# Performance work log

Measured on AMD Instinct MI355X. Metric: run time of the kernel, lower is better.

The kernel has to match this reference:

```python
import jax, jax.numpy as jnp
import numpy as np

DROPOUT_P = 0.0  # undefined global `dropout_p` in source; pinned to 0 (identity) for determinism


def setup_inputs() -> dict:
    key = jax.random.key(0)
    k1, k2, k3 = jax.random.split(key, 3)
    B, Lq, Lk, D = 16, 4096, 4096, 64
    return {
        "query": jax.random.normal(k1, (B, Lq, D), dtype=jnp.float32),
        "key": jax.random.normal(k2, (B, Lk, D), dtype=jnp.float32),
        "value": jax.random.normal(k3, (B, Lk, D), dtype=jnp.float32),
        "scale_factor": jnp.ones((1,), dtype=jnp.float32),
    }


def reference(query, key, value, scale_factor):
    # scores: [B, Lq, Lk] -- the large HBM-materialized intermediate
    scores = jnp.einsum("bqd,bkd->bqk", query, key) / scale_factor
    probs = jax.nn.softmax(scores, axis=-1)
    # dropout with p = DROPOUT_P = 0.0 is the identity
    out = jnp.einsum("bqk,bkd->bqd", probs, value)
    return out
```

## Files before the change

### kernel.cpp

```cpp
#include <hip/hip_runtime.h>
#include <hip/hip_fp16.h>

typedef _Float16 half2_t __attribute__((ext_vector_type(2)));
typedef _Float16 half4_t __attribute__((ext_vector_type(4)));
typedef _Float16 half8_t __attribute__((ext_vector_type(8)));
typedef float   float4_t __attribute__((ext_vector_type(4)));
typedef float  float16_t __attribute__((ext_vector_type(16)));

static __device__ __forceinline__ half2_t cvt_pk(float a, float b) {
    return __builtin_bit_cast(half2_t, __builtin_amdgcn_cvt_pkrtz(a, b));
}
static __device__ __forceinline__ half4_t cvt_pk4(float a, float b, float c, float d) {
    half2_t lo = cvt_pk(a, b), hi = cvt_pk(c, d);
    half4_t r;
    r[0] = lo[0]; r[1] = lo[1]; r[2] = hi[0]; r[3] = hi[1];
    return r;
}
static __device__ __forceinline__ half8_t cvt_pk8(const float4& a, const float4& b) {
    half4_t lo = cvt_pk4(a.x, a.y, a.z, a.w);
    half4_t hi = cvt_pk4(b.x, b.y, b.z, b.w);
    return __builtin_shufflevector(lo, hi, 0, 1, 2, 3, 4, 5, 6, 7);
}
static __device__ __forceinline__ half8_t join8(half4_t lo, half4_t hi) {
    return __builtin_shufflevector(lo, hi, 0, 1, 2, 3, 4, 5, 6, 7);
}
static __device__ __forceinline__ float f3(float a, float b, float c) {
    return fmaxf(fmaxf(a, b), c);
}

namespace {
constexpr int kB       = 16;
constexpr int kL       = 4096;
constexpr int kD       = 64;
constexpr int kQTile   = 128;
constexpr int kBK      = 64;
constexpr int kTiles   = kL / kBK;
constexpr int kSplit   = 2;
constexpr int kTilesHf = kTiles / kSplit;
constexpr int kTileH   = kBK * kD;
constexpr int kKStride = 72;
constexpr int kVStride = 72;
constexpr size_t kWsHalves = (size_t)kB * kTiles * kTileH;
constexpr size_t kOHalves  = (size_t)kB * kL * kD;
}


__global__ __launch_bounds__(256) void prep_kv(const float* __restrict__ K,
                                               const float* __restrict__ V,
                                               _Float16* __restrict__ Kws,
                                               _Float16* __restrict__ Vws)
{
    int blk = blockIdx.x;
    const int tid = threadIdx.x;
    if (blk < kB * kTiles) {
        const float* src = K + (size_t)blk * kTileH;
        _Float16* dst = Kws + (size_t)blk * kTileH;
#pragma unroll
        for (int i = 0; i < 2; ++i) {
            const int task = tid + 256 * i;
            const int row  = task >> 3;
            const int g    = task & 7;
            const int srow = (row & ~12) | ((row & 4) << 1) | ((row & 8) >> 1);
            const float* p = src + srow * kD + g * 8;
            const float4 a  = *(const float4*)p;
            const float4 b2 = *(const float4*)(p + 4);
            *(half8_t*)(dst + task * 8) = cvt_pk8(a, b2);
        }
    } else {
        blk -= kB * kTiles;
        const float* src = V + (size_t)blk * kTileH;
        _Float16* dst = Vws + (size_t)blk * kTileH;
        const int d  = tid & 63;
        const int vw = tid >> 6;
#pragma unroll
        for (int i = 0; i < 2; ++i) {
            const int c8 = vw * 2 + i;
            const int k0 = c8 * 8;
            float p[8];
#pragma unroll
            for (int j = 0; j < 8; ++j) p[j] = src[(k0 + j) * kD + d];
            half4_t lo = cvt_pk4(p[0], p[1], p[2], p[3]);
            half4_t hi = cvt_pk4(p[4], p[5], p[6], p[7]);
            *(half8_t*)(dst + (c8 * 64 + d) * 8) = join8(lo, hi);
        }
    }
}

__global__ __launch_bounds__(256, 4)
void fa_fwd(const float* __restrict__ Q, const _Float16* __restrict__ Kws,
            const _Float16* __restrict__ Vws, const float* __restrict__ scale_ptr,
            float* __restrict__ Out, _Float16* __restrict__ O2ws,
            float* __restrict__ Mlws)
{
    __shared__ __align__(16) _Float16 Ksh[2][kBK * kKStride];
    __shared__ __align__(16) _Float16 Vsh[2][kD * kVStride];

    const int tid  = threadIdx.x;
    const int wave = tid >> 6;
    const int lane = tid & 63;
    const int l31  = lane & 31;
    const int hi   = lane >> 5;

    const int b  = blockIdx.y;
    const int hf = blockIdx.z;
    const int q0 = blockIdx.x * kQTile + wave * 32;

    const int task0 = tid, task1 = tid + 256;
    const int vd = tid & 63;
    const int vw = tid >> 6;
    const int koff0 = (task0 >> 3) * kKStride + (task0 & 7) * 8;
    const int koff1 = (task1 >> 3) * kKStride + (task1 & 7) * 8;
    const int voff0 = vd * kVStride + (vw * 2 + 0) * 8;
    const int voff1 = vd * kVStride + (vw * 2 + 1) * 8;

    const float qscale = 1.4426950408889634f / scale_ptr[0];

    const float*    Qb = Q   + (size_t)b * kL * kD;
    const _Float16* Kt = Kws + ((size_t)b * kTiles + (size_t)hf * kTilesHf) * kTileH;
    const _Float16* Vt = Vws + ((size_t)b * kTiles + (size_t)hf * kTilesHf) * kTileH;

    half8_t qfrag[4];
    {
        const float* qrow = Qb + (size_t)(q0 + l31) * kD;
#pragma unroll
        for (int kd = 0; kd < 4; ++kd) {
            const float* p = qrow + kd * 16 + hi * 8;
            half8_t h;
#pragma unroll
            for (int j = 0; j < 8; ++j) h[j] = (_Float16)(p[j] * qscale);
            qfrag[kd] = h;
        }
    }

    float16_t O[2];
    O[0] = (float16_t)0.0f;
    O[1] = (float16_t)0.0f;
    float m_run = -__builtin_inff();
    float l_run = 0.0f;
    const float16_t Zc = (float16_t)0.0f;

    half8_t kp[2], vp[2];
    kp[0] = *(const half8_t*)(Kt + task0 * 8);
    kp[1] = *(const half8_t*)(Kt + task1 * 8);
    vp[0] = *(const half8_t*)(Vt + ((vw * 2 + 0) * 64 + vd) * 8);
    vp[1] = *(const half8_t*)(Vt + ((vw * 2 + 1) * 64 + vd) * 8);
    *(half8_t*)(&Ksh[0][koff0]) = kp[0];
    *(half8_t*)(&Ksh[0][koff1]) = kp[1];
    *(half8_t*)(&Vsh[0][voff0]) = vp[0];
    *(half8_t*)(&Vsh[0][voff1]) = vp[1];
    {
        const _Float16* kn = Kt + (size_t)1 * kTileH;
        const _Float16* vn = Vt + (size_t)1 * kTileH;
        kp[0] = *(const half8_t*)(kn + task0 * 8);
        kp[1] = *(const half8_t*)(kn + task1 * 8);
        vp[0] = *(const half8_t*)(vn + ((vw * 2 + 0) * 64 + vd) * 8);
        vp[1] = *(const half8_t*)(vn + ((vw * 2 + 1) * 64 + vd) * 8);
    }
    __syncthreads();

    for (int t = 0; t < kTilesHf; ++t) {
        const int cur = t & 1;
        const _Float16* Kb = Ksh[cur];
        const _Float16* Vb = Vsh[cur];
        _Float16* Kn = Ksh[cur ^ 1];
        _Float16* Vn = Vsh[cur ^ 1];

        *(half8_t*)(&Kn[koff0]) = kp[0];
        *(half8_t*)(&Kn[koff1]) = kp[1];
        *(half8_t*)(&Vn[voff0]) = vp[0];
        *(half8_t*)(&Vn[voff1]) = vp[1];

        {
            const int nt = (t + 2) & (kTilesHf - 1);
            const _Float16* kn = Kt + (size_t)nt * kTileH;
            const _Float16* vn = Vt + (size_t)nt * kTileH;
            kp[0] = *(const half8_t*)(kn + task0 * 8);
            kp[1] = *(const half8_t*)(kn + task1 * 8);
            vp[0] = *(const half8_t*)(vn + ((vw * 2 + 0) * 64 + vd) * 8);
            vp[1] = *(const half8_t*)(vn + ((vw * 2 + 1) * 64 + vd) * 8);
        }

        float16_t S0, S1;
        {
            half8_t kf0, kf1;
            kf0 = *(const half8_t*)(&Kb[(l31)      * kKStride + 0 * 16 + hi * 8]);
            kf1 = *(const half8_t*)(&Kb[(32 + l31) * kKStride + 0 * 16 + hi * 8]);
            __builtin_amdgcn_s_setprio(1);
            S0 = __builtin_amdgcn_mfma_f32_32x32x16_f16(kf0, qfrag[0], Zc, 0, 0, 0);
            S1 = __builtin_amdgcn_mfma_f32_32x32x16_f16(kf1, qfrag[0], Zc, 0, 0, 0);
#pragma unroll
            for (int kd = 1; kd < 4; ++kd) {
                kf0 = *(const half8_t*)(&Kb[(l31)      * kKStride + kd * 16 + hi * 8]);
                kf1 = *(const half8_t*)(&Kb[(32 + l31) * kKStride + kd * 16 + hi * 8]);
                S0 = __builtin_amdgcn_mfma_f32_32x32x16_f16(kf0, qfrag[kd], S0, 0, 0, 0);
                S1 = __builtin_amdgcn_mfma_f32_32x32x16_f16(kf1, qfrag[kd], S1, 0, 0, 0);
            }
            __builtin_amdgcn_s_setprio(0);
        }

        float v0 = f3(S0[0],  S0[1],  S0[2]);
        float v1 = f3(S0[3],  S0[4],  S0[5]);
        float v2 = f3(S0[6],  S0[7],  S0[8]);
        float v3 = f3(S0[9],  S0[10], S0[11]);
        float v4 = f3(S0[12], S0[13], S0[14]);
        float v5 = f3(S0[15], S1[0],  S1[1]);
        float v6 = f3(S1[2],  S1[3],  S1[4]);
        float v7 = f3(S1[5],  S1[6],  S1[7]);
        float v8 = f3(S1[8],  S1[9],  S1[10]);
        float v9 = f3(S1[11], S1[12], S1[13]);
        float w0 = f3(v0, v1, v2);
        float w1 = f3(v3, v4, v5);
        float w2 = f3(v6, v7, v8);
        float w3 = f3(v9, S1[14], S1[15]);
        float pm = fmaxf(fmaxf(w0, w1), fmaxf(w2, w3));
        pm = fmaxf(pm, __shfl_xor(pm, 32));

        const bool need = pm > m_run + 8.0f;
        if (__ballot(need)) {
            const float mn    = fmaxf(m_run, pm);
            const float alpha = __builtin_amdgcn_exp2f(m_run - mn);
            m_run = mn;
            l_run *= alpha;
#pragma unroll
            for (int r = 0; r < 16; ++r) { O[0][r] *= alpha; O[1][r] *= alpha; }
        }

#pragma unroll
        for (int r = 0; r < 16; ++r) {
            S0[r] = __builtin_amdgcn_exp2f(S0[r] - m_run);
            S1[r] = __builtin_amdgcn_exp2f(S1[r] - m_run);
        }
        half8_t pf[4];
        pf[0] = join8(cvt_pk4(S0[0],  S0[1],  S0[2],  S0[3]),
                      cvt_pk4(S0[4],  S0[5],  S0[6],  S0[7]));
        pf[1] = join8(cvt_pk4(S0[8],  S0[9],  S0[10], S0[11]),
                      cvt_pk4(S0[12], S0[13], S0[14], S0[15]));
        pf[2] = join8(cvt_pk4(S1[0],  S1[1],  S1[2],  S1[3]),
                      cvt_pk4(S1[4],  S1[5],  S1[6],  S1[7]));
        pf[3] = join8(cvt_pk4(S1[8],  S1[9],  S1[10], S1[11]),
                      cvt_pk4(S1[12], S1[13], S1[14], S1[15]));
#define A4(v,a) ((v[a] + v[(a)+1]) + (v[(a)+2] + v[(a)+3]))
        l_run += ((A4(S0, 0) + A4(S0, 4)) + (A4(S0, 8) + A4(S0, 12)))
               + ((A4(S1, 0) + A4(S1, 4)) + (A4(S1, 8) + A4(S1, 12)));
#undef A4

        __builtin_amdgcn_s_setprio(1);
#pragma unroll
        for (int kb = 0; kb < 4; ++kb) {
            const half8_t vf0 = *(const half8_t*)(
                &Vb[(l31)      * kVStride + kb * 16 + hi * 8]);
            const half8_t vf1 = *(const half8_t*)(
                &Vb[(32 + l31) * kVStride + kb * 16 + hi * 8]);
            O[0] = __builtin_amdgcn_mfma_f32_32x32x16_f16(vf0, pf[kb], O[0], 0, 0, 0);
            O[1] = __builtin_amdgcn_mfma_f32_32x32x16_f16(vf1, pf[kb], O[1], 0, 0, 0);
        }
        __builtin_amdgcn_s_setprio(0);

        __syncthreads();
    }

    l_run += __shfl_xor(l_run, 32);
    const float inv = 1.0f / l_run;
    const int   q   = q0 + l31;
    if (hf == 0) {
        float* op = Out + ((size_t)b * kL + q) * kD;
#pragma unroll
        for (int dt = 0; dt < 2; ++dt)
#pragma unroll
            for (int rr = 0; rr < 4; ++rr) {
                const int d0 = dt * 32 + rr * 8 + hi * 4;
                float4 w;
                w.x = O[dt][rr * 4 + 0] * inv;
                w.y = O[dt][rr * 4 + 1] * inv;
                w.z = O[dt][rr * 4 + 2] * inv;
                w.w = O[dt][rr * 4 + 3] * inv;
                *(float4*)(op + d0) = w;
            }
    } else {
        _Float16* op = O2ws + ((size_t)b * kL + q) * kD;
#pragma unroll
        for (int dt = 0; dt < 2; ++dt)
#pragma unroll
            for (int rr = 0; rr < 4; ++rr) {
                const int d0 = dt * 32 + rr * 8 + hi * 4;
                half4_t w = cvt_pk4(O[dt][rr * 4 + 0] * inv, O[dt][rr * 4 + 1] * inv,
                                    O[dt][rr * 4 + 2] * inv, O[dt][rr * 4 + 3] * inv);
                *(half4_t*)(op + d0) = w;
            }
    }
    if (hi == 0) {
        float2 ml; ml.x = m_run; ml.y = l_run;
        *(float2*)(Mlws + (((size_t)b * kL + q) * 2 + hf) * 2) = ml;
    }
}

__global__ __launch_bounds__(256)
void combine(float* __restrict__ Out, const _Float16* __restrict__ O2ws,
             const float* __restrict__ Mlws)
{
    const int t   = threadIdx.x;
    const int row = blockIdx.x * 16 + (t >> 4);
    const int d0  = (t & 15) * 4;

    const float m1 = Mlws[(size_t)row * 4 + 0];
    const float l1 = Mlws[(size_t)row * 4 + 1];
    const float m2 = Mlws[(size_t)row * 4 + 2];
    const float l2 = Mlws[(size_t)row * 4 + 3];

    const float m  = fmaxf(m1, m2);
    float w1 = l1 * exp2f(m1 - m);
    float w2 = l2 * exp2f(m2 - m);
    const float inv = 1.0f / (w1 + w2);
    w1 *= inv; w2 *= inv;

    float* op = Out + (size_t)row * kD + d0;
    const _Float16* o2 = O2ws + (size_t)row * kD + d0;
    float4 a = *(const float4*)op;
    const half4_t h = *(const half4_t*)o2;
    a.x = a.x * w1 + (float)h[0] * w2;
    a.y = a.y * w1 + (float)h[1] * w2;
    a.z = a.z * w1 + (float)h[2] * w2;
    a.w = a.w * w1 + (float)h[3] * w2;
    *(float4*)op = a;
}

extern "C" void kernel_launch(void* const* d_in, const int* in_sizes, int n_in,
                              void* d_out, int out_size, void* d_ws, size_t ws_size,
                              hipStream_t stream) {
    const float* Q = (const float*)d_in[0];
    const float* K = (const float*)d_in[1];
    const float* V = (const float*)d_in[2];
    const float* s = (const float*)d_in[3];
    float* out = (float*)d_out;
    _Float16* Kws  = (_Float16*)d_ws;
    _Float16* Vws  = Kws + kWsHalves;
    _Float16* O2ws = Vws + kWsHalves;
    float*    Mlws = (float*)(O2ws + kOHalves);

    prep_kv<<<dim3(2 * kB * kTiles), dim3(256), 0, stream>>>(K, V, Kws, Vws);
    fa_fwd<<<dim3(kL / kQTile, kB, kSplit), dim3(256), 0, stream>>>(Q, Kws, Vws, s, out, O2ws, Mlws);
    combine<<<dim3(kB * kL / 16), dim3(256), 0, stream>>>(out, O2ws, Mlws);
}
```

Before: 186.0 us.

## Load V fragments directly from global into registers, drop V LDS staging

V tiles are no longer staged through shared memory. Each wave loads its MFMA B-operand fragments for V straight from the pre-swizzled global workspace at the start of each tile iteration, and these loads are consumed after the QK^T and softmax work. The K LDS store and next-tile prefetch are moved after the QK MFMAs. This halves LDS footprint and LDS traffic, but each of the 4 waves now reads the full V tile from global/L2 (4x redundant), and load latency is only hidden within one iteration.

```diff
diff --git a/kernel.cpp b/kernel.cpp
--- a/kernel.cpp
+++ b/kernel.cpp
@@ -39,7 +39,6 @@
 constexpr int kTilesHf = kTiles / kSplit;
 constexpr int kTileH   = kBK * kD;
 constexpr int kKStride = 72;
-constexpr int kVStride = 72;
 constexpr size_t kWsHalves = (size_t)kB * kTiles * kTileH;
 constexpr size_t kOHalves  = (size_t)kB * kL * kD;
 }
@@ -93,7 +92,6 @@
             float* __restrict__ Mlws)
 {
     __shared__ __align__(16) _Float16 Ksh[2][kBK * kKStride];
-    __shared__ __align__(16) _Float16 Vsh[2][kD * kVStride];
 
     const int tid  = threadIdx.x;
     const int wave = tid >> 6;
@@ -106,12 +104,8 @@
     const int q0 = blockIdx.x * kQTile + wave * 32;
 
     const int task0 = tid, task1 = tid + 256;
-    const int vd = tid & 63;
-    const int vw = tid >> 6;
     const int koff0 = (task0 >> 3) * kKStride + (task0 & 7) * 8;
     const int koff1 = (task1 >> 3) * kKStride + (task1 & 7) * 8;
-    const int voff0 = vd * kVStride + (vw * 2 + 0) * 8;
-    const int voff1 = vd * kVStride + (vw * 2 + 1) * 8;
 
     const float qscale = 1.4426950408889634f / scale_ptr[0];
 
@@ -139,45 +133,27 @@
     float l_run = 0.0f;
     const float16_t Zc = (float16_t)0.0f;
 
-    half8_t kp[2], vp[2];
+    half8_t kp[2];
     kp[0] = *(const half8_t*)(Kt + task0 * 8);
     kp[1] = *(const half8_t*)(Kt + task1 * 8);
-    vp[0] = *(const half8_t*)(Vt + ((vw * 2 + 0) * 64 + vd) * 8);
-    vp[1] = *(const half8_t*)(Vt + ((vw * 2 + 1) * 64 + vd) * 8);
     *(half8_t*)(&Ksh[0][koff0]) = kp[0];
     *(half8_t*)(&Ksh[0][koff1]) = kp[1];
-    *(half8_t*)(&Vsh[0][voff0]) = vp[0];
-    *(half8_t*)(&Vsh[0][voff1]) = vp[1];
-    {
-        const _Float16* kn = Kt + (size_t)1 * kTileH;
-        const _Float16* vn = Vt + (size_t)1 * kTileH;
-        kp[0] = *(const half8_t*)(kn + task0 * 8);
-        kp[1] = *(const half8_t*)(kn + task1 * 8);
-        vp[0] = *(const half8_t*)(vn + ((vw * 2 + 0) * 64 + vd) * 8);
-        vp[1] = *(const half8_t*)(vn + ((vw * 2 + 1) * 64 + vd) * 8);
-    }
+    kp[0] = *(const half8_t*)(Kt + (size_t)kTileH + task0 * 8);
+    kp[1] = *(const half8_t*)(Kt + (size_t)kTileH + task1 * 8);
     __syncthreads();
 
     for (int t = 0; t < kTilesHf; ++t) {
         const int cur = t & 1;
         const _Float16* Kb = Ksh[cur];
-        const _Float16* Vb = Vsh[cur];
         _Float16* Kn = Ksh[cur ^ 1];
-        _Float16* Vn = Vsh[cur ^ 1];
-
-        *(half8_t*)(&Kn[koff0]) = kp[0];
-        *(half8_t*)(&Kn[koff1]) = kp[1];
-        *(half8_t*)(&Vn[voff0]) = vp[0];
-        *(half8_t*)(&Vn[voff1]) = vp[1];
-
-        {
-            const int nt = (t + 2) & (kTilesHf - 1);
-            const _Float16* kn = Kt + (size_t)nt * kTileH;
-            const _Float16* vn = Vt + (size_t)nt * kTileH;
-            kp[0] = *(const half8_t*)(kn + task0 * 8);
-            kp[1] = *(const half8_t*)(kn + task1 * 8);
-            vp[0] = *(const half8_t*)(vn + ((vw * 2 + 0) * 64 + vd) * 8);
-            vp[1] = *(const half8_t*)(vn + ((vw * 2 + 1) * 64 + vd) * 8);
+
+        const _Float16* vtile = Vt + (size_t)t * kTileH;
+        half8_t vr0[4], vr1[4];
+#pragma unroll
+        for (int kb = 0; kb < 4; ++kb) {
+            const _Float16* pch = vtile + (kb * 2 + hi) * 512;
+            vr0[kb] = *(const half8_t*)(pch + l31 * 8);
+            vr1[kb] = *(const half8_t*)(pch + (32 + l31) * 8);
         }
 
         float16_t S0, S1;
@@ -196,6 +172,15 @@
                 S1 = __builtin_amdgcn_mfma_f32_32x32x16_f16(kf1, qfrag[kd], S1, 0, 0, 0);
             }
             __builtin_amdgcn_s_setprio(0);
+        }
+
+        *(half8_t*)(&Kn[koff0]) = kp[0];
+        *(half8_t*)(&Kn[koff1]) = kp[1];
+        {
+            const int nt = (t + 2) & (kTilesHf - 1);
+            const _Float16* kn = Kt + (size_t)nt * kTileH;
+            kp[0] = *(const half8_t*)(kn + task0 * 8);
+            kp[1] = *(const half8_t*)(kn + task1 * 8);
         }
 
         float v0 = f3(S0[0],  S0[1],  S0[2]);
@@ -247,12 +232,8 @@
         __builtin_amdgcn_s_setprio(1);
 #pragma unroll
         for (int kb = 0; kb < 4; ++kb) {
-            const half8_t vf0 = *(const half8_t*)(
-                &Vb[(l31)      * kVStride + kb * 16 + hi * 8]);
-            const half8_t vf1 = *(const half8_t*)(
-                &Vb[(32 + l31) * kVStride + kb * 16 + hi * 8]);
-            O[0] = __builtin_amdgcn_mfma_f32_32x32x16_f16(vf0, pf[kb], O[0], 0, 0, 0);
-            O[1] = __builtin_amdgcn_mfma_f32_32x32x16_f16(vf1, pf[kb], O[1], 0, 0, 0);
+            O[0] = __builtin_amdgcn_mfma_f32_32x32x16_f16(vr0[kb], pf[kb], O[0], 0, 0, 0);
+            O[1] = __builtin_amdgcn_mfma_f32_32x32x16_f16(vr1[kb], pf[kb], O[1], 0, 0, 0);
         }
         __builtin_amdgcn_s_setprio(0);
 
```

New measurement: 231.4 us. +24.4%, slower.

## Software-pipeline PV MFMA of previous tile with QK MFMA of current tile

Applied to the files above, without the earlier changes.

Defers the P·V matrix multiply of each key tile into the next loop iteration, issuing it right after the Q·K^T MFMAs so matrix work overlaps the softmax math. V fragments and packed probabilities are kept in registers across iterations, and a final epilogue flushes the last tile. This aims to hide softmax/exp latency behind MFMA issue, at the cost of extra VGPR pressure that could reduce occupancy.

```diff
diff --git a/kernel.cpp b/kernel.cpp
--- a/kernel.cpp
+++ b/kernel.cpp
@@ -138,6 +138,11 @@
     float m_run = -__builtin_inff();
     float l_run = 0.0f;
     const float16_t Zc = (float16_t)0.0f;
+
+    const half8_t hz = (half8_t)(_Float16)0.0f;
+    half8_t pf[4]  = {hz, hz, hz, hz};
+    half8_t vfr0[4] = {hz, hz, hz, hz};
+    half8_t vfr1[4] = {hz, hz, hz, hz};
 
     half8_t kp[2], vp[2];
     kp[0] = *(const half8_t*)(Kt + task0 * 8);
@@ -165,11 +170,34 @@
         _Float16* Kn = Ksh[cur ^ 1];
         _Float16* Vn = Vsh[cur ^ 1];
 
+        float16_t S0, S1;
+        {
+            half8_t kf0, kf1;
+            kf0 = *(const half8_t*)(&Kb[(l31)      * kKStride + 0 * 16 + hi * 8]);
+            kf1 = *(const half8_t*)(&Kb[(32 + l31) * kKStride + 0 * 16 + hi * 8]);
+            __builtin_amdgcn_s_setprio(1);
+            S0 = __builtin_amdgcn_mfma_f32_32x32x16_f16(kf0, qfrag[0], Zc, 0, 0, 0);
+            S1 = __builtin_amdgcn_mfma_f32_32x32x16_f16(kf1, qfrag[0], Zc, 0, 0, 0);
+#pragma unroll
+            for (int kd = 1; kd < 4; ++kd) {
+                kf0 = *(const half8_t*)(&Kb[(l31)      * kKStride + kd * 16 + hi * 8]);
+                kf1 = *(const half8_t*)(&Kb[(32 + l31) * kKStride + kd * 16 + hi * 8]);
+                S0 = __builtin_amdgcn_mfma_f32_32x32x16_f16(kf0, qfrag[kd], S0, 0, 0, 0);
+                S1 = __builtin_amdgcn_mfma_f32_32x32x16_f16(kf1, qfrag[kd], S1, 0, 0, 0);
+            }
+#pragma unroll
+            for (int kb = 0; kb < 4; ++kb)
+                O[0] = __builtin_amdgcn_mfma_f32_32x32x16_f16(vfr0[kb], pf[kb], O[0], 0, 0, 0);
+#pragma unroll
+            for (int kb = 0; kb < 4; ++kb)
+                O[1] = __builtin_amdgcn_mfma_f32_32x32x16_f16(vfr1[kb], pf[kb], O[1], 0, 0, 0);
+            __builtin_amdgcn_s_setprio(0);
+        }
+
         *(half8_t*)(&Kn[koff0]) = kp[0];
         *(half8_t*)(&Kn[koff1]) = kp[1];
         *(half8_t*)(&Vn[voff0]) = vp[0];
         *(half8_t*)(&Vn[voff1]) = vp[1];
-
         {
             const int nt = (t + 2) & (kTilesHf - 1);
             const _Float16* kn = Kt + (size_t)nt * kTileH;
@@ -178,24 +206,6 @@
             kp[1] = *(const half8_t*)(kn + task1 * 8);
             vp[0] = *(const half8_t*)(vn + ((vw * 2 + 0) * 64 + vd) * 8);
             vp[1] = *(const half8_t*)(vn + ((vw * 2 + 1) * 64 + vd) * 8);
-        }
-
-        float16_t S0, S1;
-        {
-            half8_t kf0, kf1;
-            kf0 = *(const half8_t*)(&Kb[(l31)      * kKStride + 0 * 16 + hi * 8]);
-            kf1 = *(const half8_t*)(&Kb[(32 + l31) * kKStride + 0 * 16 + hi * 8]);
-            __builtin_amdgcn_s_setprio(1);
-            S0 = __builtin_amdgcn_mfma_f32_32x32x16_f16(kf0, qfrag[0], Zc, 0, 0, 0);
-            S1 = __builtin_amdgcn_mfma_f32_32x32x16_f16(kf1, qfrag[0], Zc, 0, 0, 0);
-#pragma unroll
-            for (int kd = 1; kd < 4; ++kd) {
-                kf0 = *(const half8_t*)(&Kb[(l31)      * kKStride + kd * 16 + hi * 8]);
-                kf1 = *(const half8_t*)(&Kb[(32 + l31) * kKStride + kd * 16 + hi * 8]);
-                S0 = __builtin_amdgcn_mfma_f32_32x32x16_f16(kf0, qfrag[kd], S0, 0, 0, 0);
-                S1 = __builtin_amdgcn_mfma_f32_32x32x16_f16(kf1, qfrag[kd], S1, 0, 0, 0);
-            }
-            __builtin_amdgcn_s_setprio(0);
         }
 
         float v0 = f3(S0[0],  S0[1],  S0[2]);
@@ -230,34 +240,37 @@
             S0[r] = __builtin_amdgcn_exp2f(S0[r] - m_run);
             S1[r] = __builtin_amdgcn_exp2f(S1[r] - m_run);
         }
-        half8_t pf[4];
+
         pf[0] = join8(cvt_pk4(S0[0],  S0[1],  S0[2],  S0[3]),
                       cvt_pk4(S0[4],  S0[5],  S0[6],  S0[7]));
         pf[1] = join8(cvt_pk4(S0[8],  S0[9],  S0[10], S0[11]),
                       cvt_pk4(S0[12], S0[13], S0[14], S0[15]));
+#pragma unroll
+        for (int kb = 0; kb < 4; ++kb)
+            vfr0[kb] = *(const half8_t*)(&Vb[(l31) * kVStride + kb * 16 + hi * 8]);
         pf[2] = join8(cvt_pk4(S1[0],  S1[1],  S1[2],  S1[3]),
                       cvt_pk4(S1[4],  S1[5],  S1[6],  S1[7]));
         pf[3] = join8(cvt_pk4(S1[8],  S1[9],  S1[10], S1[11]),
                       cvt_pk4(S1[12], S1[13], S1[14], S1[15]));
+#pragma unroll
+        for (int kb = 0; kb < 4; ++kb)
+            vfr1[kb] = *(const half8_t*)(&Vb[(32 + l31) * kVStride + kb * 16 + hi * 8]);
 #define A4(v,a) ((v[a] + v[(a)+1]) + (v[(a)+2] + v[(a)+3]))
         l_run += ((A4(S0, 0) + A4(S0, 4)) + (A4(S0, 8) + A4(S0, 12)))
                + ((A4(S1, 0) + A4(S1, 4)) + (A4(S1, 8) + A4(S1, 12)));
 #undef A4
 
-        __builtin_amdgcn_s_setprio(1);
-#pragma unroll
-        for (int kb = 0; kb < 4; ++kb) {
-            const half8_t vf0 = *(const half8_t*)(
-                &Vb[(l31)      * kVStride + kb * 16 + hi * 8]);
-            const half8_t vf1 = *(const half8_t*)(
-                &Vb[(32 + l31) * kVStride + kb * 16 + hi * 8]);
-            O[0] = __builtin_amdgcn_mfma_f32_32x32x16_f16(vf0, pf[kb], O[0], 0, 0, 0);
-            O[1] = __builtin_amdgcn_mfma_f32_32x32x16_f16(vf1, pf[kb], O[1], 0, 0, 0);
-        }
-        __builtin_amdgcn_s_setprio(0);
-
         __syncthreads();
     }
+
+    __builtin_amdgcn_s_setprio(1);
+#pragma unroll
+    for (int kb = 0; kb < 4; ++kb)
+        O[0] = __builtin_amdgcn_mfma_f32_32x32x16_f16(vfr0[kb], pf[kb], O[0], 0, 0, 0);
+#pragma unroll
+    for (int kb = 0; kb < 4; ++kb)
+        O[1] = __builtin_amdgcn_mfma_f32_32x32x16_f16(vfr1[kb], pf[kb], O[1], 0, 0, 0);
+    __builtin_amdgcn_s_setprio(0);
 
     l_run += __shfl_xor(l_run, 32);
     const float inv = 1.0f / l_run;
```

Result: slower. 337.6 us (+81.5%).

## Fuse split-K combine into attention kernel via last-arriver atomic flag

Applied to the files above, without the earlier changes.

Removes the separate combine kernel launch. Each attention block increments a per-(batch, q-tile) counter after writing its partial output and max/sum stats, and the second block to finish merges the two halves in place. This saves a kernel launch and its pass over the output, but adds a memset, threadfences and an atomic, and leaves the merge running on only one of the two blocks per tile.

```diff
diff --git a/kernel.cpp b/kernel.cpp
--- a/kernel.cpp
+++ b/kernel.cpp
@@ -40,6 +40,7 @@
 constexpr int kTileH   = kBK * kD;
 constexpr int kKStride = 72;
 constexpr int kVStride = 72;
+constexpr int kQB      = kL / kQTile;
 constexpr size_t kWsHalves = (size_t)kB * kTiles * kTileH;
 constexpr size_t kOHalves  = (size_t)kB * kL * kD;
 }
@@ -90,10 +91,11 @@
 void fa_fwd(const float* __restrict__ Q, const _Float16* __restrict__ Kws,
             const _Float16* __restrict__ Vws, const float* __restrict__ scale_ptr,
             float* __restrict__ Out, _Float16* __restrict__ O2ws,
-            float* __restrict__ Mlws)
+            float* __restrict__ Mlws, int* __restrict__ Flags)
 {
     __shared__ __align__(16) _Float16 Ksh[2][kBK * kKStride];
     __shared__ __align__(16) _Float16 Vsh[2][kD * kVStride];
+    __shared__ int role;
 
     const int tid  = threadIdx.x;
     const int wave = tid >> 6;
@@ -292,36 +294,40 @@
         float2 ml; ml.x = m_run; ml.y = l_run;
         *(float2*)(Mlws + (((size_t)b * kL + q) * 2 + hf) * 2) = ml;
     }
-}
-
-__global__ __launch_bounds__(256)
-void combine(float* __restrict__ Out, const _Float16* __restrict__ O2ws,
-             const float* __restrict__ Mlws)
-{
-    const int t   = threadIdx.x;
-    const int row = blockIdx.x * 16 + (t >> 4);
-    const int d0  = (t & 15) * 4;
-
-    const float m1 = Mlws[(size_t)row * 4 + 0];
-    const float l1 = Mlws[(size_t)row * 4 + 1];
-    const float m2 = Mlws[(size_t)row * 4 + 2];
-    const float l2 = Mlws[(size_t)row * 4 + 3];
-
-    const float m  = fmaxf(m1, m2);
-    float w1 = l1 * exp2f(m1 - m);
-    float w2 = l2 * exp2f(m2 - m);
-    const float inv = 1.0f / (w1 + w2);
-    w1 *= inv; w2 *= inv;
-
-    float* op = Out + (size_t)row * kD + d0;
-    const _Float16* o2 = O2ws + (size_t)row * kD + d0;
-    float4 a = *(const float4*)op;
-    const half4_t h = *(const half4_t*)o2;
-    a.x = a.x * w1 + (float)h[0] * w2;
-    a.y = a.y * w1 + (float)h[1] * w2;
-    a.z = a.z * w1 + (float)h[2] * w2;
-    a.w = a.w * w1 + (float)h[3] * w2;
-    *(float4*)op = a;
+
+    __syncthreads();
+    if (tid == 0) {
+        __threadfence();
+        role = atomicAdd(&Flags[b * kQB + blockIdx.x], 1);
+    }
+    __syncthreads();
+    if (role == 1) {
+        __threadfence();
+        const int r  = tid >> 1;
+        const int dh = (tid & 1) * 32;
+        const size_t rowg = (size_t)b * kL + blockIdx.x * kQTile + r;
+        const float m1 = Mlws[rowg * 4 + 0];
+        const float l1 = Mlws[rowg * 4 + 1];
+        const float m2 = Mlws[rowg * 4 + 2];
+        const float l2 = Mlws[rowg * 4 + 3];
+        const float mm = fmaxf(m1, m2);
+        float w1 = l1 * __builtin_amdgcn_exp2f(m1 - mm);
+        float w2 = l2 * __builtin_amdgcn_exp2f(m2 - mm);
+        const float winv = 1.0f / (w1 + w2);
+        w1 *= winv; w2 *= winv;
+        float* op = Out + rowg * kD + dh;
+        const _Float16* o2 = O2ws + rowg * kD + dh;
+#pragma unroll
+        for (int j = 0; j < 8; ++j) {
+            float4 a = *(const float4*)(op + j * 4);
+            const half4_t h = *(const half4_t*)(o2 + j * 4);
+            a.x = a.x * w1 + (float)h[0] * w2;
+            a.y = a.y * w1 + (float)h[1] * w2;
+            a.z = a.z * w1 + (float)h[2] * w2;
+            a.w = a.w * w1 + (float)h[3] * w2;
+            *(float4*)(op + j * 4) = a;
+        }
+    }
 }
 
 extern "C" void kernel_launch(void* const* d_in, const int* in_sizes, int n_in,
@@ -336,8 +342,9 @@
     _Float16* Vws  = Kws + kWsHalves;
     _Float16* O2ws = Vws + kWsHalves;
     float*    Mlws = (float*)(O2ws + kOHalves);
-
+    int*      Flags = (int*)(Mlws + (size_t)kB * kL * 4);
+
+    hipMemsetAsync(Flags, 0, kB * kQB * sizeof(int), stream);
     prep_kv<<<dim3(2 * kB * kTiles), dim3(256), 0, stream>>>(K, V, Kws, Vws);
-    fa_fwd<<<dim3(kL / kQTile, kB, kSplit), dim3(256), 0, stream>>>(Q, Kws, Vws, s, out, O2ws, Mlws);
-    combine<<<dim3(kB * kL / 16), dim3(256), 0, stream>>>(out, O2ws, Mlws);
-}
+    fa_fwd<<<dim3(kQB, kB, kSplit), dim3(256), 0, stream>>>(Q, Kws, Vws, s, out, O2ws, Mlws, Flags);
+}
```

After: 298.3 us. +60.4%, slower.
